# Kernel tuning notes

Hardware: AMD Instinct MI355X
Metric: run time of the kernel (lower is better)

Reference implementation:

```python
import jax, jax.numpy as jnp
import numpy as np

HEADS = 16
SEQ_LEN = 2048
EMB = 1024
BATCH = 2


def setup_inputs() -> dict:
    key = jax.random.key(0)
    ks = jax.random.split(key, 5)
    s = 1.0 / np.sqrt(EMB)
    return {
        "x": jax.random.normal(ks[0], (BATCH, SEQ_LEN, EMB), dtype=jnp.float32),
        "Wk": jax.random.normal(ks[1], (EMB, EMB), dtype=jnp.float32) * s,
        "Wq": jax.random.normal(ks[2], (EMB, EMB), dtype=jnp.float32) * s,
        "Wv": jax.random.normal(ks[3], (EMB, EMB), dtype=jnp.float32) * s,
        "Wu": jax.random.normal(ks[4], (EMB, EMB), dtype=jnp.float32) * s,
        "bu": jnp.zeros((EMB,), dtype=jnp.float32),
    }


def reference(x, Wk, Wq, Wv, Wu, bu):
    B, S, E = x.shape
    H = HEADS
    D = E // H
    # projections (torch Linear: y = x @ W.T); split heads -> [B, H, S, D]
    def proj(W):
        return (x @ W.T).reshape(B, S, H, D).transpose(0, 2, 1, 3)
    q, k, v = proj(Wq), proj(Wk), proj(Wv)
    scores = jnp.einsum("bhsd,bhtd->bhst", q, k) / jnp.sqrt(jnp.float32(D))
    causal_mask = jnp.triu(jnp.ones((S, S), dtype=bool), k=1)  # True above diag
    scores = jnp.where(causal_mask, -jnp.inf, scores)
    attn = jax.nn.softmax(scores, axis=-1)
    ctx = jnp.einsum("bhst,bhtd->bhsd", attn, v)  # [B,H,S,D]
    out = ctx.transpose(0, 2, 1, 3).reshape(B, S, E)
    return out @ Wu.T + bu
```

## Files before the change

kernel.cpp:

```cpp
#include <hip/hip_runtime.h>
#include <hip/hip_bf16.h>

#define HEADS 16
#define SEQ   2048
#define EMB   1024
#define BATCH 2
#define DHEAD 64
#define MTOK  (BATCH * SEQ)

typedef __bf16 bf16x8 __attribute__((ext_vector_type(8)));
typedef float  floatx4 __attribute__((ext_vector_type(4)));

#if __has_builtin(__builtin_amdgcn_exp2f)
#define EXP2(x) __builtin_amdgcn_exp2f(x)
#else
#define EXP2(x) exp2f(x)
#endif

__device__ __forceinline__ void gl_lds16(const void* g, void* l) {
  __builtin_amdgcn_global_load_lds((__attribute__((address_space(1))) void*)(g),
                                   (__attribute__((address_space(3))) void*)(l), 16, 0, 0);
}

__device__ __forceinline__ unsigned short f2bf(float f) {
  __bf16 h = (__bf16)f;
  return __builtin_bit_cast(unsigned short, h);
}

__global__ __launch_bounds__(256) void cvt_kernel(
    const float* __restrict__ x,  const float* __restrict__ wq,
    const float* __restrict__ wk, const float* __restrict__ wv,
    const float* __restrict__ wu,
    unsigned short* __restrict__ xb,  unsigned short* __restrict__ wqb,
    unsigned short* __restrict__ wkb, unsigned short* __restrict__ wvb,
    unsigned short* __restrict__ wub) {
  const int g = blockIdx.x * 256 + threadIdx.x;
  const int XG = (MTOK * EMB) / 4;
  const int WG = (EMB * EMB) / 4;
  const float* src; unsigned short* dst; int off;
  if (g < XG) { src = x; dst = xb; off = g; }
  else {
    int t = g - XG; int wsel = t / WG; off = t - wsel * WG;
    const float* ss[4] = {wq, wk, wv, wu};
    unsigned short* dd[4] = {wqb, wkb, wvb, wub};
    src = ss[wsel]; dst = dd[wsel];
  }
  float4 v = ((const float4*)src)[off];
  ushort4 o;
  o.x = f2bf(v.x); o.y = f2bf(v.y); o.z = f2bf(v.z); o.w = f2bf(v.w);
  ((ushort4*)dst)[off] = o;
}

__global__ __launch_bounds__(256) void gemm_qkv(
    const unsigned short* __restrict__ xb,
    const unsigned short* __restrict__ wqb, const unsigned short* __restrict__ wkb,
    const unsigned short* __restrict__ wvb,
    unsigned short* __restrict__ Qb, unsigned short* __restrict__ Kb,
    unsigned short* __restrict__ Vt) {
  constexpr int BM = 128, BN = 128, BK = 32;
  __shared__ unsigned short As[BM * BK];
  __shared__ unsigned short Bs[BN * BK];
  const int z = blockIdx.z;
  const unsigned short* W = (z == 0) ? wqb : (z == 1) ? wkb : wvb;
  const int m0 = blockIdx.x * BM, n0 = blockIdx.y * BN;
  const int tid = threadIdx.x, w = tid >> 6, lane = tid & 63;
  const int quad = lane >> 4, l16 = lane & 15;
  const int wm = w >> 1, wn = w & 1;
  const int srow = lane >> 2, skoff = (lane & 3) * 8;

  floatx4 acc[4][4] = {};

  for (int kt = 0; kt < EMB / BK; ++kt) {
    const int k0 = kt * BK;
#pragma unroll
    for (int i = 0; i < BM / 64; ++i) {
      int r = i * 64 + w * 16;
      gl_lds16(xb + (size_t)(m0 + r + srow) * EMB + k0 + skoff, &As[r * BK]);
    }
#pragma unroll
    for (int i = 0; i < BN / 64; ++i) {
      int r = i * 64 + w * 16;
      gl_lds16(W + (size_t)(n0 + r + srow) * EMB + k0 + skoff, &Bs[r * BK]);
    }
    __syncthreads();
    bf16x8 af[4], bfv[4];
#pragma unroll
    for (int mb = 0; mb < 4; ++mb)
      af[mb] = *(const bf16x8*)&As[(wm * 64 + mb * 16 + l16) * BK + quad * 8];
#pragma unroll
    for (int nb = 0; nb < 4; ++nb)
      bfv[nb] = *(const bf16x8*)&Bs[(wn * 64 + nb * 16 + l16) * BK + quad * 8];
#pragma unroll
    for (int mb = 0; mb < 4; ++mb)
#pragma unroll
      for (int nb = 0; nb < 4; ++nb)
        acc[mb][nb] = __builtin_amdgcn_mfma_f32_16x16x32_bf16(af[mb], bfv[nb], acc[mb][nb], 0, 0, 0);
    __syncthreads();
  }

  if (z < 2) {
    unsigned short* C = (z == 0) ? Qb : Kb;
    const float scale = (z == 0) ? 0.180336876f : 1.0f;
#pragma unroll
    for (int mb = 0; mb < 4; ++mb) {
#pragma unroll
      for (int nb = 0; nb < 4; ++nb) {
        int n = n0 + wn * 64 + nb * 16 + l16;
#pragma unroll
        for (int r = 0; r < 4; ++r) {
          int m = m0 + wm * 64 + mb * 16 + quad * 4 + r;
          C[(size_t)m * EMB + n] = f2bf(acc[mb][nb][r] * scale);
        }
      }
    }
  } else {
#pragma unroll
    for (int mb = 0; mb < 4; ++mb) {
      int mbase = m0 + wm * 64 + mb * 16 + quad * 4;
      int b = mbase >> 11, s = mbase & (SEQ - 1);
#pragma unroll
      for (int nb = 0; nb < 4; ++nb) {
        int n = n0 + wn * 64 + nb * 16 + l16;
        ushort4 o;
        o.x = f2bf(acc[mb][nb][0]); o.y = f2bf(acc[mb][nb][1]);
        o.z = f2bf(acc[mb][nb][2]); o.w = f2bf(acc[mb][nb][3]);
        *(ushort4*)&Vt[((size_t)b * (HEADS * DHEAD) + n) * SEQ + s] = o;
      }
    }
  }
}

__global__ __launch_bounds__(256) void attn_kernel(
    const unsigned short* __restrict__ Qb, const unsigned short* __restrict__ Kb,
    const unsigned short* __restrict__ Vt, unsigned short* __restrict__ ctx) {
  constexpr int KT = 128;
  constexpr int PST = KT + 8;
  __shared__ unsigned short Ks[KT * DHEAD];
  __shared__ unsigned short Vs[DHEAD * KT];
  __shared__ __bf16 Ps[4 * 16 * PST];
  const int pair = blockIdx.x, bh = blockIdx.y;
  const int b = bh >> 4, h = bh & 15;
  const int tid = threadIdx.x, w = tid >> 6, lane = tid & 63;
  const int quad = lane >> 4, l16 = lane & 15;

  const unsigned short* Kbh = Kb + (size_t)b * SEQ * EMB + h * DHEAD;
  const unsigned short* Vbh = Vt + (size_t)bh * DHEAD * SEQ;
  __bf16* Pw = &Ps[w * (16 * PST)];

  int kq[4], kd[4], vd[4], vk[4];
#pragma unroll
  for (int i = 0; i < 4; ++i) {
    int c = i * 256 + tid;
    kq[i] = ((c >> 6) & 7) * 16 + (c & 15);
    kd[i] = ((c >> 9) << 5) + (((c >> 4) & 3) << 3);
    vd[i] = (((c >> 6) & 3) << 4) + (c & 15);
    vk[i] = (((c >> 8) & 3) << 5) + (((c >> 4) & 3) << 3);
  }

  for (int pi = 0; pi < 2; ++pi) {
    const int qt = pi ? (31 - pair) : pair;
    const int q0 = qt * 64;
    const int myrow = q0 + w * 16 + quad * 4;

    const size_t qrow = (size_t)(b * SEQ + q0 + w * 16 + l16) * EMB + h * DHEAD;
    bf16x8 qf[2];
    qf[0] = *(const bf16x8*)&Qb[qrow + quad * 8];
    qf[1] = *(const bf16x8*)&Qb[qrow + 32 + quad * 8];

    float mrow[4], lrow[4];
    floatx4 acc_o[4] = {};
#pragma unroll
    for (int r = 0; r < 4; ++r) { mrow[r] = -1e30f; lrow[r] = 0.0f; }

    const int nkt = (qt + 2) >> 1;
    for (int ktile = 0; ktile < nkt; ++ktile) {
      const int kt0 = ktile * KT;
#pragma unroll
      for (int i = 0; i < 4; ++i) {
        gl_lds16(Kbh + (size_t)(kt0 + kq[i]) * EMB + kd[i], &Ks[(i * 256 + w * 64) * 8]);
        gl_lds16(Vbh + (size_t)vd[i] * SEQ + kt0 + vk[i], &Vs[(i * 256 + w * 64) * 8]);
      }
      __syncthreads();

      floatx4 accs[8] = {};
#pragma unroll
      for (int ks = 0; ks < 2; ++ks)
#pragma unroll
        for (int nb = 0; nb < 8; ++nb) {
          bf16x8 kf = *(const bf16x8*)&Ks[((ks * 8 + nb) * 64 + lane) * 8];
          accs[nb] = __builtin_amdgcn_mfma_f32_16x16x32_bf16(qf[ks], kf, accs[nb], 0, 0, 0);
        }

      const bool diag = (ktile == nkt - 1);
#pragma unroll
      for (int r = 0; r < 4; ++r) {
        float sv[8];
#pragma unroll
        for (int nb = 0; nb < 8; ++nb) sv[nb] = accs[nb][r];
        if (diag) {
          int row = myrow + r;
#pragma unroll
          for (int nb = 0; nb < 8; ++nb) {
            int col = kt0 + nb * 16 + l16;
            if (col > row) sv[nb] = -1e30f;
          }
        }
        float rm = sv[0];
#pragma unroll
        for (int nb = 1; nb < 8; ++nb) rm = fmaxf(rm, sv[nb]);
        rm = fmaxf(rm, __shfl_xor(rm, 1));
        rm = fmaxf(rm, __shfl_xor(rm, 2));
        rm = fmaxf(rm, __shfl_xor(rm, 4));
        rm = fmaxf(rm, __shfl_xor(rm, 8));
        float mnew = fmaxf(mrow[r], rm);
        float alpha = EXP2(mrow[r] - mnew);
        float rs = 0.0f;
#pragma unroll
        for (int nb = 0; nb < 8; ++nb) {
          float pe = EXP2(sv[nb] - mnew);
          Pw[(quad * 4 + r) * PST + nb * 16 + l16] = (__bf16)pe;
          rs += pe;
        }
        rs += __shfl_xor(rs, 1);
        rs += __shfl_xor(rs, 2);
        rs += __shfl_xor(rs, 4);
        rs += __shfl_xor(rs, 8);
        lrow[r] = lrow[r] * alpha + rs;
        mrow[r] = mnew;
#pragma unroll
        for (int nb = 0; nb < 4; ++nb) acc_o[nb][r] *= alpha;
      }

#pragma unroll
      for (int ks = 0; ks < 4; ++ks) {
        bf16x8 pf = *(const bf16x8*)&Pw[l16 * PST + ks * 32 + quad * 8];
#pragma unroll
        for (int nb = 0; nb < 4; ++nb) {
          bf16x8 vf = *(const bf16x8*)&Vs[((ks * 4 + nb) * 64 + lane) * 8];
          acc_o[nb] = __builtin_amdgcn_mfma_f32_16x16x32_bf16(pf, vf, acc_o[nb], 0, 0, 0);
        }
      }
      __syncthreads();
    }

#pragma unroll
    for (int r = 0; r < 4; ++r) {
      float inv = 1.0f / lrow[r];
      size_t base = (size_t)(b * SEQ + myrow + r) * EMB + h * DHEAD;
#pragma unroll
      for (int nb = 0; nb < 4; ++nb)
        ctx[base + nb * 16 + l16] = f2bf(acc_o[nb][r] * inv);
    }
  }
}

__global__ __launch_bounds__(256) void gemm_out(
    const unsigned short* __restrict__ ctx, const unsigned short* __restrict__ wub,
    const float* __restrict__ bu, float* __restrict__ out) {
  constexpr int BM = 128, BN = 64, BK = 32;
  __shared__ unsigned short As[BM * BK];
  __shared__ unsigned short Bs[BN * BK];
  const int m0 = blockIdx.x * BM, n0 = blockIdx.y * BN;
  const int tid = threadIdx.x, w = tid >> 6, lane = tid & 63;
  const int quad = lane >> 4, l16 = lane & 15;
  const int wm = w >> 1, wn = w & 1;
  const int srow = lane >> 2, skoff = (lane & 3) * 8;

  floatx4 acc[4][2] = {};

  for (int kt = 0; kt < EMB / BK; ++kt) {
    const int k0 = kt * BK;
#pragma unroll
    for (int i = 0; i < 2; ++i) {
      int r = i * 64 + w * 16;
      gl_lds16(ctx + (size_t)(m0 + r + srow) * EMB + k0 + skoff, &As[r * BK]);
    }
    gl_lds16(wub + (size_t)(n0 + w * 16 + srow) * EMB + k0 + skoff, &Bs[(w * 16) * BK]);
    __syncthreads();
    bf16x8 af[4], bfv[2];
#pragma unroll
    for (int mb = 0; mb < 4; ++mb)
      af[mb] = *(const bf16x8*)&As[(wm * 64 + mb * 16 + l16) * BK + quad * 8];
#pragma unroll
    for (int nb = 0; nb < 2; ++nb)
      bfv[nb] = *(const bf16x8*)&Bs[(wn * 32 + nb * 16 + l16) * BK + quad * 8];
#pragma unroll
    for (int mb = 0; mb < 4; ++mb)
#pragma unroll
      for (int nb = 0; nb < 2; ++nb)
        acc[mb][nb] = __builtin_amdgcn_mfma_f32_16x16x32_bf16(af[mb], bfv[nb], acc[mb][nb], 0, 0, 0);
    __syncthreads();
  }

#pragma unroll
  for (int mb = 0; mb < 4; ++mb) {
#pragma unroll
    for (int nb = 0; nb < 2; ++nb) {
      int n = n0 + wn * 32 + nb * 16 + l16;
      float bias = bu[n];
#pragma unroll
      for (int r = 0; r < 4; ++r) {
        int m = m0 + wm * 64 + mb * 16 + quad * 4 + r;
        out[(size_t)m * EMB + n] = acc[mb][nb][r] + bias;
      }
    }
  }
}

extern "C" void kernel_launch(void* const* d_in, const int* in_sizes, int n_in,
                              void* d_out, int out_size, void* d_ws, size_t ws_size,
                              hipStream_t stream) {
  const float* x  = (const float*)d_in[0];
  const float* Wk = (const float*)d_in[1];
  const float* Wq = (const float*)d_in[2];
  const float* Wv = (const float*)d_in[3];
  const float* Wu = (const float*)d_in[4];
  const float* bu = (const float*)d_in[5];

  char* ws = (char*)d_ws;
  const size_t MB1 = 1 << 20;
  unsigned short* xb  = (unsigned short*)(ws + 0);
  unsigned short* wqb = (unsigned short*)(ws + 8  * MB1);
  unsigned short* wkb = (unsigned short*)(ws + 10 * MB1);
  unsigned short* wvb = (unsigned short*)(ws + 12 * MB1);
  unsigned short* wub = (unsigned short*)(ws + 14 * MB1);
  unsigned short* Qb  = (unsigned short*)(ws + 16 * MB1);
  unsigned short* Kb  = (unsigned short*)(ws + 24 * MB1);
  unsigned short* Vt  = (unsigned short*)(ws + 32 * MB1);
  unsigned short* ctx = (unsigned short*)(ws + 40 * MB1);

  cvt_kernel<<<8192, 256, 0, stream>>>(x, Wq, Wk, Wv, Wu, xb, wqb, wkb, wvb, wub);
  gemm_qkv<<<dim3(32, 8, 3), 256, 0, stream>>>(xb, wqb, wkb, wvb, Qb, Kb, Vt);
  attn_kernel<<<dim3(16, 32), 256, 0, stream>>>(Qb, Kb, Vt, ctx);
  gemm_out<<<dim3(32, 16), 256, 0, stream>>>(ctx, wub, bu, (float*)d_out);
}
```

Baseline: 200.4 us.

## Transpose attention MFMA so each lane owns one query row, one tile per block

The attention kernel swaps MFMA operand order so scores come out transposed. Each lane then holds a whole query row's values in registers, and the row max and sum need only two cross-lane shuffles instead of per-row 4-step reductions. P and the output are written as packed ushort4 stores. The paired query-tile scheme is dropped: each block now handles one query tile, the grid doubles, and heavy tiles are scheduled first. exp2 is now the plain exp2f call rather than the builtin, which may cost extra instructions.

```diff
diff --git a/kernel.cpp b/kernel.cpp
--- a/kernel.cpp
+++ b/kernel.cpp
@@ -10,12 +10,6 @@
 
 typedef __bf16 bf16x8 __attribute__((ext_vector_type(8)));
 typedef float  floatx4 __attribute__((ext_vector_type(4)));
-
-#if __has_builtin(__builtin_amdgcn_exp2f)
-#define EXP2(x) __builtin_amdgcn_exp2f(x)
-#else
-#define EXP2(x) exp2f(x)
-#endif
 
 __device__ __forceinline__ void gl_lds16(const void* g, void* l) {
   __builtin_amdgcn_global_load_lds((__attribute__((address_space(1))) void*)(g),
@@ -137,15 +131,16 @@
   constexpr int PST = KT + 8;
   __shared__ unsigned short Ks[KT * DHEAD];
   __shared__ unsigned short Vs[DHEAD * KT];
-  __shared__ __bf16 Ps[4 * 16 * PST];
-  const int pair = blockIdx.x, bh = blockIdx.y;
+  __shared__ unsigned short Ps[4 * 16 * PST];
+  const int qt = 31 - blockIdx.x, bh = blockIdx.y;
   const int b = bh >> 4, h = bh & 15;
+  const int q0 = qt * 64;
   const int tid = threadIdx.x, w = tid >> 6, lane = tid & 63;
   const int quad = lane >> 4, l16 = lane & 15;
 
   const unsigned short* Kbh = Kb + (size_t)b * SEQ * EMB + h * DHEAD;
   const unsigned short* Vbh = Vt + (size_t)bh * DHEAD * SEQ;
-  __bf16* Pw = &Ps[w * (16 * PST)];
+  unsigned short* Pw = &Ps[w * (16 * PST)];
 
   int kq[4], kd[4], vd[4], vk[4];
 #pragma unroll
@@ -157,100 +152,95 @@
     vk[i] = (((c >> 8) & 3) << 5) + (((c >> 4) & 3) << 3);
   }
 
-  for (int pi = 0; pi < 2; ++pi) {
-    const int qt = pi ? (31 - pair) : pair;
-    const int q0 = qt * 64;
-    const int myrow = q0 + w * 16 + quad * 4;
-
-    const size_t qrow = (size_t)(b * SEQ + q0 + w * 16 + l16) * EMB + h * DHEAD;
-    bf16x8 qf[2];
-    qf[0] = *(const bf16x8*)&Qb[qrow + quad * 8];
-    qf[1] = *(const bf16x8*)&Qb[qrow + 32 + quad * 8];
-
-    float mrow[4], lrow[4];
-    floatx4 acc_o[4] = {};
-#pragma unroll
-    for (int r = 0; r < 4; ++r) { mrow[r] = -1e30f; lrow[r] = 0.0f; }
-
-    const int nkt = (qt + 2) >> 1;
-    for (int ktile = 0; ktile < nkt; ++ktile) {
-      const int kt0 = ktile * KT;
-#pragma unroll
-      for (int i = 0; i < 4; ++i) {
-        gl_lds16(Kbh + (size_t)(kt0 + kq[i]) * EMB + kd[i], &Ks[(i * 256 + w * 64) * 8]);
-        gl_lds16(Vbh + (size_t)vd[i] * SEQ + kt0 + vk[i], &Vs[(i * 256 + w * 64) * 8]);
-      }
-      __syncthreads();
-
-      floatx4 accs[8] = {};
-#pragma unroll
-      for (int ks = 0; ks < 2; ++ks)
-#pragma unroll
-        for (int nb = 0; nb < 8; ++nb) {
-          bf16x8 kf = *(const bf16x8*)&Ks[((ks * 8 + nb) * 64 + lane) * 8];
-          accs[nb] = __builtin_amdgcn_mfma_f32_16x16x32_bf16(qf[ks], kf, accs[nb], 0, 0, 0);
-        }
-
-      const bool diag = (ktile == nkt - 1);
-#pragma unroll
-      for (int r = 0; r < 4; ++r) {
-        float sv[8];
-#pragma unroll
-        for (int nb = 0; nb < 8; ++nb) sv[nb] = accs[nb][r];
-        if (diag) {
-          int row = myrow + r;
-#pragma unroll
-          for (int nb = 0; nb < 8; ++nb) {
-            int col = kt0 + nb * 16 + l16;
-            if (col > row) sv[nb] = -1e30f;
-          }
-        }
-        float rm = sv[0];
-#pragma unroll
-        for (int nb = 1; nb < 8; ++nb) rm = fmaxf(rm, sv[nb]);
-        rm = fmaxf(rm, __shfl_xor(rm, 1));
-        rm = fmaxf(rm, __shfl_xor(rm, 2));
-        rm = fmaxf(rm, __shfl_xor(rm, 4));
-        rm = fmaxf(rm, __shfl_xor(rm, 8));
-        float mnew = fmaxf(mrow[r], rm);
-        float alpha = EXP2(mrow[r] - mnew);
-        float rs = 0.0f;
-#pragma unroll
-        for (int nb = 0; nb < 8; ++nb) {
-          float pe = EXP2(sv[nb] - mnew);
-          Pw[(quad * 4 + r) * PST + nb * 16 + l16] = (__bf16)pe;
-          rs += pe;
-        }
-        rs += __shfl_xor(rs, 1);
-        rs += __shfl_xor(rs, 2);
-        rs += __shfl_xor(rs, 4);
-        rs += __shfl_xor(rs, 8);
-        lrow[r] = lrow[r] * alpha + rs;
-        mrow[r] = mnew;
-#pragma unroll
-        for (int nb = 0; nb < 4; ++nb) acc_o[nb][r] *= alpha;
-      }
-
-#pragma unroll
-      for (int ks = 0; ks < 4; ++ks) {
-        bf16x8 pf = *(const bf16x8*)&Pw[l16 * PST + ks * 32 + quad * 8];
-#pragma unroll
-        for (int nb = 0; nb < 4; ++nb) {
-          bf16x8 vf = *(const bf16x8*)&Vs[((ks * 4 + nb) * 64 + lane) * 8];
-          acc_o[nb] = __builtin_amdgcn_mfma_f32_16x16x32_bf16(pf, vf, acc_o[nb], 0, 0, 0);
-        }
-      }
-      __syncthreads();
-    }
-
-#pragma unroll
-    for (int r = 0; r < 4; ++r) {
-      float inv = 1.0f / lrow[r];
-      size_t base = (size_t)(b * SEQ + myrow + r) * EMB + h * DHEAD;
-#pragma unroll
-      for (int nb = 0; nb < 4; ++nb)
-        ctx[base + nb * 16 + l16] = f2bf(acc_o[nb][r] * inv);
-    }
+  const int myq = q0 + w * 16 + l16;
+  const size_t qrow = (size_t)(b * SEQ + myq) * EMB + h * DHEAD;
+  bf16x8 qf[2];
+  qf[0] = *(const bf16x8*)&Qb[qrow + quad * 8];
+  qf[1] = *(const bf16x8*)&Qb[qrow + 32 + quad * 8];
+
+  float mrow = -1e30f, lrow = 0.0f;
+  floatx4 acc_o[4] = {};
+
+  const int nkt = (qt + 2) >> 1;
+  for (int ktile = 0; ktile < nkt; ++ktile) {
+    const int kt0 = ktile * KT;
+#pragma unroll
+    for (int i = 0; i < 4; ++i) {
+      gl_lds16(Kbh + (size_t)(kt0 + kq[i]) * EMB + kd[i], &Ks[(i * 256 + w * 64) * 8]);
+      gl_lds16(Vbh + (size_t)vd[i] * SEQ + kt0 + vk[i], &Vs[(i * 256 + w * 64) * 8]);
+    }
+    __syncthreads();
+
+    floatx4 accs[8] = {};
+#pragma unroll
+    for (int ks = 0; ks < 2; ++ks)
+#pragma unroll
+      for (int nb = 0; nb < 8; ++nb) {
+        bf16x8 kf = *(const bf16x8*)&Ks[((ks * 8 + nb) * 64 + lane) * 8];
+        accs[nb] = __builtin_amdgcn_mfma_f32_16x16x32_bf16(kf, qf[ks], accs[nb], 0, 0, 0);
+      }
+
+    if (ktile == nkt - 1) {
+#pragma unroll
+      for (int nb = 0; nb < 8; ++nb) {
+        int kbase = kt0 + nb * 16 + quad * 4;
+#pragma unroll
+        for (int r = 0; r < 4; ++r)
+          if (kbase + r > myq) accs[nb][r] = -1e30f;
+      }
+    }
+
+    float rm = -1e30f;
+#pragma unroll
+    for (int nb = 0; nb < 8; ++nb) {
+      float t0 = fmaxf(fmaxf(accs[nb][0], accs[nb][1]), fmaxf(accs[nb][2], accs[nb][3]));
+      rm = fmaxf(rm, t0);
+    }
+    rm = fmaxf(rm, __shfl_xor(rm, 16));
+    rm = fmaxf(rm, __shfl_xor(rm, 32));
+    const float mnew = fmaxf(mrow, rm);
+    const float alpha = exp2f(mrow - mnew);
+    float rs = 0.0f;
+#pragma unroll
+    for (int nb = 0; nb < 8; ++nb) {
+      float p0 = exp2f(accs[nb][0] - mnew);
+      float p1 = exp2f(accs[nb][1] - mnew);
+      float p2 = exp2f(accs[nb][2] - mnew);
+      float p3 = exp2f(accs[nb][3] - mnew);
+      rs += (p0 + p1) + (p2 + p3);
+      ushort4 pk;
+      pk.x = f2bf(p0); pk.y = f2bf(p1); pk.z = f2bf(p2); pk.w = f2bf(p3);
+      *(ushort4*)&Pw[l16 * PST + nb * 16 + quad * 4] = pk;
+    }
+    rs += __shfl_xor(rs, 16);
+    rs += __shfl_xor(rs, 32);
+    lrow = lrow * alpha + rs;
+    mrow = mnew;
+#pragma unroll
+    for (int nb = 0; nb < 4; ++nb)
+#pragma unroll
+      for (int r = 0; r < 4; ++r) acc_o[nb][r] *= alpha;
+
+#pragma unroll
+    for (int ks = 0; ks < 4; ++ks) {
+      bf16x8 pf = *(const bf16x8*)&Pw[l16 * PST + ks * 32 + quad * 8];
+#pragma unroll
+      for (int nb = 0; nb < 4; ++nb) {
+        bf16x8 vf = *(const bf16x8*)&Vs[((ks * 4 + nb) * 64 + lane) * 8];
+        acc_o[nb] = __builtin_amdgcn_mfma_f32_16x16x32_bf16(vf, pf, acc_o[nb], 0, 0, 0);
+      }
+    }
+    __syncthreads();
+  }
+
+  const float inv = 1.0f / lrow;
+  const size_t obase = (size_t)(b * SEQ + myq) * EMB + h * DHEAD;
+#pragma unroll
+  for (int nb = 0; nb < 4; ++nb) {
+    ushort4 o;
+    o.x = f2bf(acc_o[nb][0] * inv); o.y = f2bf(acc_o[nb][1] * inv);
+    o.z = f2bf(acc_o[nb][2] * inv); o.w = f2bf(acc_o[nb][3] * inv);
+    *(ushort4*)&ctx[obase + nb * 16 + quad * 4] = o;
   }
 }
 
@@ -331,6 +321,6 @@
 
   cvt_kernel<<<8192, 256, 0, stream>>>(x, Wq, Wk, Wv, Wu, xb, wqb, wkb, wvb, wub);
   gemm_qkv<<<dim3(32, 8, 3), 256, 0, stream>>>(xb, wqb, wkb, wvb, Qb, Kb, Vt);
-  attn_kernel<<<dim3(16, 32), 256, 0, stream>>>(Qb, Kb, Vt, ctx);
+  attn_kernel<<<dim3(32, 32), 256, 0, stream>>>(Qb, Kb, Vt, ctx);
   gemm_out<<<dim3(32, 16), 256, 0, stream>>>(ctx, wub, bu, (float*)d_out);
 }
```

New measurement: 240.4 us. 1.2x slower.
